# Kernel optimization log

Hardware: AMD Instinct MI355X
Metric: run time of the kernel (lower is better)

The kernel has to match this reference:

```python
import jax, jax.numpy as jnp
import numpy as np

NEG_SLOPE = 0.2  # PyG GATConv default LeakyReLU slope
NUM_GRAPHS = 64


def gat_layer(x, src, dst, W, a_src, a_dst, b, concat):
    """PyG GATConv (eval mode, add_self_loops=True).
    x: [N, F_in]; W: [F_in, H*C]; a_src,a_dst: [H, C]; b: [H*C] or [C].
    """
    N = x.shape[0]
    H, C = a_src.shape
    h = (x @ W).reshape(N, H, C)                      # [N, H, C]
    # add self-loops
    loop = jnp.arange(N, dtype=src.dtype)
    s = jnp.concatenate([src, loop])                  # [E+N]
    d = jnp.concatenate([dst, loop])
    al_s = jnp.einsum('nhc,hc->nh', h, a_src)         # [N, H]
    al_d = jnp.einsum('nhc,hc->nh', h, a_dst)
    e = jax.nn.leaky_relu(al_s[s] + al_d[d], NEG_SLOPE)   # [E+N, H]
    # segment softmax over incoming edges per destination node
    m = jax.ops.segment_max(e, d, num_segments=N)     # [N, H]
    ex = jnp.exp(e - m[d])
    denom = jax.ops.segment_sum(ex, d, num_segments=N)
    alpha = ex / denom[d]                             # [E+N, H]
    msg = h[s] * alpha[:, :, None]                    # [E+N, H, C]
    out = jax.ops.segment_sum(msg, d, num_segments=N) # [N, H, C]
    out = out.reshape(N, H * C) if concat else out.mean(axis=1)
    return out + b


def setup_inputs() -> dict:
    key = jax.random.key(0)
    ks = jax.random.split(key, 16)
    N, E, F_in, Hid, Out = 50000, 800000, 128, 64, 10
    x = jax.random.normal(ks[0], (N, F_in), dtype=jnp.float32)
    edge_index = jax.random.randint(ks[1], (2, E), 0, N, dtype=jnp.int32)
    batch = jnp.sort(jax.random.randint(ks[2], (N,), 0, NUM_GRAPHS, dtype=jnp.int32))

    def glorot(k, shape):
        fan = shape[0] + shape[-1]
        return jax.random.normal(k, shape, dtype=jnp.float32) * np.sqrt(2.0 / fan)

    H1 = 8
    params = dict(
        W1=glorot(ks[3], (F_in, H1 * Hid)), a1_src=glorot(ks[4], (H1, Hid)),
        a1_dst=glorot(ks[5], (H1, Hid)), b1=jnp.zeros((H1 * Hid,), jnp.float32),
        W2=glorot(ks[6], (H1 * Hid, Hid)), a2_src=glorot(ks[7], (1, Hid)),
        a2_dst=glorot(ks[8], (1, Hid)), b2=jnp.zeros((Hid,), jnp.float32),
        W3=glorot(ks[9], (Hid, Hid)), a3_src=glorot(ks[10], (1, Hid)),
        a3_dst=glorot(ks[11], (1, Hid)), b3=jnp.zeros((Hid,), jnp.float32),
        fc_W=glorot(ks[12], (Hid, Out)), fc_b=jnp.zeros((Out,), jnp.float32),
    )
    return dict(x=x, edge_index=edge_index, batch=batch, **params)


def reference(x, edge_index, batch,
              W1, a1_src, a1_dst, b1,
              W2, a2_src, a2_dst, b2,
              W3, a3_src, a3_dst, b3,
              fc_W, fc_b):
    src, dst = edge_index[0], edge_index[1]
    # dropout is a no-op in eval mode
    h = jax.nn.elu(gat_layer(x, src, dst, W1, a1_src, a1_dst, b1, concat=True))
    h = jax.nn.elu(gat_layer(h, src, dst, W2, a2_src, a2_dst, b2, concat=False))
    h = jax.nn.elu(gat_layer(h, src, dst, W3, a3_src, a3_dst, b3, concat=False))
    # global mean pool over graphs
    sums = jax.ops.segment_sum(h, batch, num_segments=NUM_GRAPHS)
    cnts = jax.ops.segment_sum(jnp.ones((h.shape[0], 1), h.dtype), batch,
                               num_segments=NUM_GRAPHS)
    pooled = sums / jnp.maximum(cnts, 1.0)
    return pooled @ fc_W + fc_b
```

## Files before the change

kernel.cpp:

```cpp
#include <hip/hip_runtime.h>
#include <hip/hip_bf16.h>
#include <cstdint>

#define NEG_SLOPE 0.2f

typedef __attribute__((ext_vector_type(8))) short bf16x8;
typedef __attribute__((ext_vector_type(4))) float f32x4;

__device__ __forceinline__ float bf2f(uint32_t u) {
  union { float f; uint32_t i; } v;
  v.i = u << 16;
  return v.f;
}
__device__ __forceinline__ float lo16(uint32_t u) {
  union { float f; uint32_t i; } v;
  v.i = u << 16;
  return v.f;
}
__device__ __forceinline__ float hi16(uint32_t u) {
  union { float f; uint32_t i; } v;
  v.i = u & 0xffff0000u;
  return v.f;
}
__device__ __forceinline__ ushort f2bf(float f) {
  union { float f; uint32_t i; } v;
  v.f = f;
  uint32_t r = v.i + 0x7FFF + ((v.i >> 16) & 1);
  return (ushort)(r >> 16);
}

__global__ void prep_kernel(const float4* __restrict__ x,
                            uint2* __restrict__ x_bf, int n_x4,
                            const float* __restrict__ W1,
                            ushort* __restrict__ W1T,
                            const float* __restrict__ W2,
                            ushort* __restrict__ W2T,
                            const float* __restrict__ W3,
                            ushort* __restrict__ W3T,
                            const int* __restrict__ dst, int* __restrict__ cnt,
                            const float* __restrict__ a1s,
                            const float* __restrict__ a1d,
                            float* __restrict__ at_s, float* __restrict__ at_d,
                            int E) {
  int i = blockIdx.x * 256 + threadIdx.x;
  const int r0 = n_x4;
  const int r1 = r0 + 512 * 128;
  const int r2 = r1 + 64 * 512;
  const int r3 = r2 + 64 * 64;
  const int r4 = r3 + E;
  const int r5 = r4 + 1024;
  const int r6 = r5 + 1024;
  if (i < r0) {
    float4 v = x[i];
    uint2 o;
    o.x = (uint32_t)f2bf(v.x) | ((uint32_t)f2bf(v.y) << 16);
    o.y = (uint32_t)f2bf(v.z) | ((uint32_t)f2bf(v.w) << 16);
    x_bf[i] = o;
  } else if (i < r1) {
    int idx = i - r0;
    int n = idx >> 7, k = idx & 127;
    W1T[idx] = f2bf(W1[(size_t)k * 512 + n]);
  } else if (i < r2) {
    int idx = i - r1;
    int n = idx >> 9, k = idx & 511;
    W2T[idx] = f2bf(W2[(size_t)k * 64 + n]);
  } else if (i < r3) {
    int idx = i - r2;
    int n = idx >> 6, k = idx & 63;
    W3T[idx] = f2bf(W3[(size_t)k * 64 + n]);
  } else if (i < r4) {
    atomicAdd(&cnt[dst[i - r3]], 1);
  } else if (i < r5) {
    int idx = i - r4;
    int k = idx >> 3, h = idx & 7;
    float a = 0.f;
    for (int c = 0; c < 64; ++c)
      a = fmaf(W1[(size_t)k * 512 + h * 64 + c], a1s[h * 64 + c], a);
    at_s[idx] = a;
  } else if (i < r6) {
    int idx = i - r5;
    int k = idx >> 3, h = idx & 7;
    float a = 0.f;
    for (int c = 0; c < 64; ++c)
      a = fmaf(W1[(size_t)k * 512 + h * 64 + c], a1d[h * 64 + c], a);
    at_d[idx] = a;
  }
}

__global__ __launch_bounds__(256) void algemm_kernel(
    const ushort* __restrict__ x_bf, const float* __restrict__ at_s,
    const float* __restrict__ at_d, float* __restrict__ al_s,
    float* __restrict__ al_d, int Nn) {
  const int n = blockIdx.x * 256 + threadIdx.x;
  if (n >= Nn) return;
  float as8[8] = {}, ad8[8] = {};
  const ushort* xp = x_bf + (size_t)n * 128;
  for (int k0 = 0; k0 < 128; k0 += 8) {
    const uint4 xw = *(const uint4*)(xp + k0);
    const uint32_t ww0 = xw.x, ww1 = xw.y, ww2 = xw.z, ww3 = xw.w;
    float xv[8];
    xv[0] = lo16(ww0); xv[1] = hi16(ww0);
    xv[2] = lo16(ww1); xv[3] = hi16(ww1);
    xv[4] = lo16(ww2); xv[5] = hi16(ww2);
    xv[6] = lo16(ww3); xv[7] = hi16(ww3);
#pragma unroll
    for (int t = 0; t < 8; ++t) {
      const int k = k0 + t;
#pragma unroll
      for (int h = 0; h < 8; ++h) {
        as8[h] = fmaf(xv[t], at_s[k * 8 + h], as8[h]);
        ad8[h] = fmaf(xv[t], at_d[k * 8 + h], ad8[h]);
      }
    }
  }
  float4* ps = (float4*)(al_s + (size_t)n * 8);
  ps[0] = make_float4(as8[0], as8[1], as8[2], as8[3]);
  ps[1] = make_float4(as8[4], as8[5], as8[6], as8[7]);
  float4* pd = (float4*)(al_d + (size_t)n * 8);
  pd[0] = make_float4(ad8[0], ad8[1], ad8[2], ad8[3]);
  pd[1] = make_float4(ad8[4], ad8[5], ad8[6], ad8[7]);
}

__global__ __launch_bounds__(256) void gemm_n64_al(
    const ushort* __restrict__ A, const ushort* __restrict__ BT,
    ushort* __restrict__ C, const float* __restrict__ asrc,
    const float* __restrict__ adst, float* __restrict__ al_s,
    float* __restrict__ al_d, int M, int K) {
  const int wave = threadIdx.x >> 6;
  const int lane = threadIdx.x & 63;
  const int rt = blockIdx.y * 4 + wave;
  const int r0 = rt * 16;
  if (r0 >= M) return;
  const int l15 = lane & 15, q = lane >> 4;
  const ushort* Ap = A + (size_t)(r0 + l15) * K + q * 8;
  f32x4 acc[4] = {};
  for (int k0 = 0; k0 < K; k0 += 32) {
    bf16x8 a = *(const bf16x8*)(Ap + k0);
#pragma unroll
    for (int j = 0; j < 4; ++j) {
      const bf16x8 b =
          *(const bf16x8*)(BT + (size_t)(j * 16 + l15) * K + q * 8 + k0);
      acc[j] = __builtin_amdgcn_mfma_f32_16x16x32_bf16(a, b, acc[j], 0, 0, 0);
    }
  }
#pragma unroll
  for (int j = 0; j < 4; ++j)
#pragma unroll
    for (int r = 0; r < 4; ++r) {
      int row = r0 + q * 4 + r;
      C[(size_t)row * 64 + j * 16 + l15] = f2bf(acc[j][r]);
    }
  float als_p[4] = {0.f, 0.f, 0.f, 0.f};
  float ald_p[4] = {0.f, 0.f, 0.f, 0.f};
#pragma unroll
  for (int j = 0; j < 4; ++j) {
    float wsc = asrc[j * 16 + l15];
    float wdc = adst[j * 16 + l15];
#pragma unroll
    for (int r = 0; r < 4; ++r) {
      als_p[r] = fmaf(acc[j][r], wsc, als_p[r]);
      ald_p[r] = fmaf(acc[j][r], wdc, ald_p[r]);
    }
  }
#pragma unroll
  for (int r = 0; r < 4; ++r) {
    float vs = als_p[r], vd = ald_p[r];
#pragma unroll
    for (int off = 1; off < 16; off <<= 1) {
      vs += __shfl_xor(vs, off);
      vd += __shfl_xor(vd, off);
    }
    if (l15 == 0) {
      int row = r0 + q * 4 + r;
      al_s[row] = vs;
      al_d[row] = vd;
    }
  }
}

__global__ __launch_bounds__(256) void gemm1h_kernel(
    const ushort* __restrict__ A, const ushort* __restrict__ BT,
    const float* __restrict__ b1, ushort* __restrict__ C, int M) {
  const int wave = threadIdx.x >> 6;
  const int lane = threadIdx.x & 63;
  const int rt = blockIdx.y * 4 + wave;
  const int r0 = rt * 16;
  if (r0 >= M) return;
  const int hd = blockIdx.x;
  const int l15 = lane & 15, q = lane >> 4;
  const ushort* Ap = A + (size_t)(r0 + l15) * 1024 + hd * 128 + q * 8;
  f32x4 acc[4] = {};
  for (int k0 = 0; k0 < 128; k0 += 32) {
    bf16x8 a = *(const bf16x8*)(Ap + k0);
#pragma unroll
    for (int j = 0; j < 4; ++j) {
      const bf16x8 b = *(const bf16x8*)(BT + (size_t)(hd * 64 + j * 16 + l15) * 128 +
                                        q * 8 + k0);
      acc[j] = __builtin_amdgcn_mfma_f32_16x16x32_bf16(a, b, acc[j], 0, 0, 0);
    }
  }
#pragma unroll
  for (int j = 0; j < 4; ++j)
#pragma unroll
    for (int r = 0; r < 4; ++r) {
      const int row = r0 + q * 4 + r;
      const int col = hd * 64 + j * 16 + l15;
      float v = acc[j][r] + b1[col];
      v = (v > 0.f) ? v : __expf(v) - 1.f;
      C[(size_t)row * 512 + col] = f2bf(v);
    }
}

__global__ void scan_block(const int* __restrict__ in, int* __restrict__ out,
                           int* __restrict__ bsum, int n) {
  __shared__ int sm[256];
  int gid = blockIdx.x * 256 + threadIdx.x;
  int v = (gid < n) ? in[gid] : 0;
  sm[threadIdx.x] = v;
  __syncthreads();
  for (int off = 1; off < 256; off <<= 1) {
    int t = (threadIdx.x >= off) ? sm[threadIdx.x - off] : 0;
    __syncthreads();
    sm[threadIdx.x] += t;
    __syncthreads();
  }
  if (gid < n) out[gid] = sm[threadIdx.x];
  if (threadIdx.x == 255) bsum[blockIdx.x] = sm[255];
}

__global__ void scan_final2(const int* __restrict__ inc,
                            const int* __restrict__ bsum,
                            int* __restrict__ indptr, int* __restrict__ fill,
                            int n) {
  __shared__ int sm[256];
  const int t = threadIdx.x, bx = blockIdx.x;
  sm[t] = (t < bx) ? bsum[t] : 0;
  __syncthreads();
  for (int off = 128; off; off >>= 1) {
    if (t < off) sm[t] += sm[t + off];
    __syncthreads();
  }
  const int prefix = sm[0];
  int gid = bx * 256 + t;
  if (gid < n) {
    int val = inc[gid] + prefix;
    indptr[gid + 1] = val;
    fill[gid + 1] = val;
  }
  if (gid == 0) {
    indptr[0] = 0;
    fill[0] = 0;
  }
}

__global__ void scatter_kernel(const int* __restrict__ src,
                               const int* __restrict__ dst,
                               int* __restrict__ fill,
                               int* __restrict__ csr_src, int E) {
  int e = blockIdx.x * 256 + threadIdx.x;
  if (e < E) {
    int pos = atomicAdd(&fill[dst[e]], 1);
    csr_src[pos] = src[e];
  }
}

__global__ __launch_bounds__(256) void attn1x_kernel(
    const int* __restrict__ indptr, const int* __restrict__ csr_src,
    const float* __restrict__ al_s, const float* __restrict__ al_d,
    const ushort* __restrict__ x_bf, ushort* __restrict__ agg, int Nn) {
  __shared__ float u_sm[4][64 * 8];
  __shared__ int s_sm[4][64];
  const int wv = threadIdx.x >> 6;
  const int l = threadIdx.x & 63;
  const int w = (blockIdx.x * 256 + threadIdx.x) >> 6;
  if (w >= Nn) return;
  const int d = w;
  const int start = indptr[d];
  const int deg = indptr[d + 1] - start;
  const int total = deg + 1;
  const float4 ad0 = *(const float4*)(al_d + (size_t)d * 8);
  const float4 ad1 = *(const float4*)(al_d + (size_t)d * 8 + 4);
  const ushort* xcol = x_bf + l * 2;

  float acc0[8] = {};
  float acc1[8] = {};
  float den8[8] = {};
  float* usm = u_sm[wv];
  int* ssm = s_sm[wv];

  for (int e0 = 0; e0 < total; e0 += 64) {
    const int e = e0 + l;
    int s_l = d;
    float u8[8] = {};
    if (e < total) {
      s_l = (e < deg) ? csr_src[start + e] : d;
      const float4 s0 = *(const float4*)(al_s + (size_t)s_l * 8);
      const float4 s1 = *(const float4*)(al_s + (size_t)s_l * 8 + 4);
      float vv[8];
      vv[0] = s0.x + ad0.x; vv[1] = s0.y + ad0.y;
      vv[2] = s0.z + ad0.z; vv[3] = s0.w + ad0.w;
      vv[4] = s1.x + ad1.x; vv[5] = s1.y + ad1.y;
      vv[6] = s1.z + ad1.z; vv[7] = s1.w + ad1.w;
#pragma unroll
      for (int k = 0; k < 8; ++k) {
        float v = fmaxf(vv[k], NEG_SLOPE * vv[k]);
        u8[k] = __expf(v);
        den8[k] += u8[k];
      }
    }
    ssm[l] = s_l;
    ((float4*)(usm + l * 8))[0] = make_float4(u8[0], u8[1], u8[2], u8[3]);
    ((float4*)(usm + l * 8))[1] = make_float4(u8[4], u8[5], u8[6], u8[7]);

    const int ne = min(64, total - e0);
#pragma unroll 4
    for (int j = 0; j < ne; ++j) {
      const int s = ssm[j];
      const float4 ua = *((const float4*)(usm + j * 8));
      const float4 ub = *((const float4*)(usm + j * 8) + 1);
      const uint32_t wx = *(const uint32_t*)(xcol + (size_t)s * 128);
      const float xlo = lo16(wx);
      const float xhi = hi16(wx);
      acc0[0] = fmaf(ua.x, xlo, acc0[0]); acc1[0] = fmaf(ua.x, xhi, acc1[0]);
      acc0[1] = fmaf(ua.y, xlo, acc0[1]); acc1[1] = fmaf(ua.y, xhi, acc1[1]);
      acc0[2] = fmaf(ua.z, xlo, acc0[2]); acc1[2] = fmaf(ua.z, xhi, acc1[2]);
      acc0[3] = fmaf(ua.w, xlo, acc0[3]); acc1[3] = fmaf(ua.w, xhi, acc1[3]);
      acc0[4] = fmaf(ub.x, xlo, acc0[4]); acc1[4] = fmaf(ub.x, xhi, acc1[4]);
      acc0[5] = fmaf(ub.y, xlo, acc0[5]); acc1[5] = fmaf(ub.y, xhi, acc1[5]);
      acc0[6] = fmaf(ub.z, xlo, acc0[6]); acc1[6] = fmaf(ub.z, xhi, acc1[6]);
      acc0[7] = fmaf(ub.w, xlo, acc0[7]); acc1[7] = fmaf(ub.w, xhi, acc1[7]);
    }
  }
#pragma unroll
  for (int k = 0; k < 8; ++k) {
#pragma unroll
    for (int off = 1; off < 64; off <<= 1) den8[k] += __shfl_xor(den8[k], off);
  }
  ushort* op = agg + (size_t)d * 1024 + l * 2;
#pragma unroll
  for (int h = 0; h < 8; ++h) {
    const float inv = 1.f / den8[h];
    const uint32_t st = (uint32_t)f2bf(acc0[h] * inv) |
                        ((uint32_t)f2bf(acc1[h] * inv) << 16);
    *(uint32_t*)(op + h * 128) = st;
  }
}

__global__ __launch_bounds__(256) void attn_h1_kernel(
    const int* __restrict__ indptr, const int* __restrict__ csr_src,
    const float* __restrict__ al_s, const float* __restrict__ al_d,
    const ushort* __restrict__ hin, const float* __restrict__ bias,
    ushort* __restrict__ outp, int Nn) {
  const int w = (blockIdx.x * 256 + threadIdx.x) >> 6;
  const int l = threadIdx.x & 63;
  if (w >= Nn) return;
  const int d = w;
  const int start = indptr[d];
  const int deg = indptr[d + 1] - start;
  const int total = deg + 1;
  const int t = l >> 3;
  const int c8 = l & 7;
  const float ald = al_d[d];
  const ushort* hl = hin + c8 * 8;

  float acc[8] = {0.f, 0.f, 0.f, 0.f, 0.f, 0.f, 0.f, 0.f};
  float den = 0.f;

  for (int e0 = 0; e0 < total; e0 += 64) {
    const int e = e0 + l;
    int s_l = d;
    float u_l = 0.f;
    if (e < total) {
      s_l = (e < deg) ? csr_src[start + e] : d;
      float v = al_s[s_l] + ald;
      v = fmaxf(v, NEG_SLOPE * v);
      u_l = __expf(v);
      den += u_l;
    }
    const int ne = min(64, total - e0);
    int su0 = __shfl(s_l, t);
    float uv0 = __shfl(u_l, t);
    uint4 h0 = *(const uint4*)(hl + (size_t)su0 * 64);
    int j = 0;
    for (; j + 8 < ne; j += 8) {
      const int su1 = __shfl(s_l, j + 8 + t);
      const float uv1 = __shfl(u_l, j + 8 + t);
      const uint4 h1v = *(const uint4*)(hl + (size_t)su1 * 64);
      acc[0] = fmaf(uv0, lo16(h0.x), acc[0]);
      acc[1] = fmaf(uv0, hi16(h0.x), acc[1]);
      acc[2] = fmaf(uv0, lo16(h0.y), acc[2]);
      acc[3] = fmaf(uv0, hi16(h0.y), acc[3]);
      acc[4] = fmaf(uv0, lo16(h0.z), acc[4]);
      acc[5] = fmaf(uv0, hi16(h0.z), acc[5]);
      acc[6] = fmaf(uv0, lo16(h0.w), acc[6]);
      acc[7] = fmaf(uv0, hi16(h0.w), acc[7]);
      uv0 = uv1;
      h0 = h1v;
    }
    acc[0] = fmaf(uv0, lo16(h0.x), acc[0]);
    acc[1] = fmaf(uv0, hi16(h0.x), acc[1]);
    acc[2] = fmaf(uv0, lo16(h0.y), acc[2]);
    acc[3] = fmaf(uv0, hi16(h0.y), acc[3]);
    acc[4] = fmaf(uv0, lo16(h0.z), acc[4]);
    acc[5] = fmaf(uv0, hi16(h0.z), acc[5]);
    acc[6] = fmaf(uv0, lo16(h0.w), acc[6]);
    acc[7] = fmaf(uv0, hi16(h0.w), acc[7]);
  }
#pragma unroll
  for (int k = 0; k < 8; ++k) {
    acc[k] += __shfl_xor(acc[k], 8);
    acc[k] += __shfl_xor(acc[k], 16);
    acc[k] += __shfl_xor(acc[k], 32);
  }
#pragma unroll
  for (int off = 32; off; off >>= 1) den += __shfl_xor(den, off);
  const float inv = 1.f / den;
  if (l < 8) {
    float o[8];
#pragma unroll
    for (int k = 0; k < 8; ++k) {
      float v = acc[k] * inv + bias[l * 8 + k];
      o[k] = (v > 0.f) ? v : __expf(v) - 1.f;
    }
    uint4 st;
    st.x = (uint32_t)f2bf(o[0]) | ((uint32_t)f2bf(o[1]) << 16);
    st.y = (uint32_t)f2bf(o[2]) | ((uint32_t)f2bf(o[3]) << 16);
    st.z = (uint32_t)f2bf(o[4]) | ((uint32_t)f2bf(o[5]) << 16);
    st.w = (uint32_t)f2bf(o[6]) | ((uint32_t)f2bf(o[7]) << 16);
    *(uint4*)(outp + (size_t)d * 64 + l * 8) = st;
  }
}

__global__ __launch_bounds__(256) void pool_fc_kernel(
    const ushort* __restrict__ out3, const int* __restrict__ batch, int Nn,
    const float* __restrict__ fcW, const float* __restrict__ fcb,
    float* __restrict__ out) {
  __shared__ int bnds[2];
  __shared__ float sm[4 * 64];
  __shared__ float pm[64];
  const int tid = threadIdx.x;
  const int g = blockIdx.x;
  if (tid < 2) {
    int target = g + tid;
    int lo = 0, hi = Nn;
    while (lo < hi) {
      int mid = (lo + hi) >> 1;
      if (batch[mid] < target) lo = mid + 1; else hi = mid;
    }
    bnds[tid] = lo;
  }
  __syncthreads();
  const int lb = bnds[0], ub = bnds[1];

  const int ro = tid >> 3, c8 = tid & 7;
  float acc[8] = {0.f, 0.f, 0.f, 0.f, 0.f, 0.f, 0.f, 0.f};
  for (int r = lb + ro; r < ub; r += 32) {
    const uint4 hh4 = *(const uint4*)(out3 + (size_t)r * 64 + c8 * 8);
    acc[0] += lo16(hh4.x);
    acc[1] += hi16(hh4.x);
    acc[2] += lo16(hh4.y);
    acc[3] += hi16(hh4.y);
    acc[4] += lo16(hh4.z);
    acc[5] += hi16(hh4.z);
    acc[6] += lo16(hh4.w);
    acc[7] += hi16(hh4.w);
  }
#pragma unroll
  for (int k = 0; k < 8; ++k) {
    acc[k] += __shfl_xor(acc[k], 8);
    acc[k] += __shfl_xor(acc[k], 16);
    acc[k] += __shfl_xor(acc[k], 32);
  }
  const int wv = tid >> 6, ll = tid & 63;
  if (ll < 8) {
#pragma unroll
    for (int k = 0; k < 8; ++k) sm[wv * 64 + ll * 8 + k] = acc[k];
  }
  __syncthreads();
  if (tid < 64) {
    float tot = sm[tid] + sm[64 + tid] + sm[128 + tid] + sm[192 + tid];
    pm[tid] = tot / fmaxf((float)(ub - lb), 1.f);
  }
  __syncthreads();
  if (tid < 10) {
    float a = fcb[tid];
    for (int c = 0; c < 64; ++c) a = fmaf(pm[c], fcW[c * 10 + tid], a);
    out[g * 10 + tid] = a;
  }
}

extern "C" void kernel_launch(void* const* d_in, const int* in_sizes, int n_in,
                              void* d_out, int out_size, void* d_ws,
                              size_t ws_size, hipStream_t stream) {
  const float* x = (const float*)d_in[0];
  const int* ei = (const int*)d_in[1];
  const int* batch = (const int*)d_in[2];
  const float* W1 = (const float*)d_in[3];
  const float* a1s = (const float*)d_in[4];
  const float* a1d = (const float*)d_in[5];
  const float* b1 = (const float*)d_in[6];
  const float* W2 = (const float*)d_in[7];
  const float* a2s = (const float*)d_in[8];
  const float* a2d = (const float*)d_in[9];
  const float* b2 = (const float*)d_in[10];
  const float* W3 = (const float*)d_in[11];
  const float* a3s = (const float*)d_in[12];
  const float* a3d = (const float*)d_in[13];
  const float* b3 = (const float*)d_in[14];
  const float* fcW = (const float*)d_in[15];
  const float* fcb = (const float*)d_in[16];
  float* out = (float*)d_out;

  const int N = in_sizes[0] / 128;
  const int E = in_sizes[1] / 2;
  const int* srcp = ei;
  const int* dstp = ei + E;

  char* ws = (char*)d_ws;
  size_t off = 0;
  auto alloc = [&](size_t bytes) -> void* {
    off = (off + 255) & ~(size_t)255;
    void* p = ws + off;
    off += bytes;
    return p;
  };
  ushort* x_bf = (ushort*)alloc((size_t)N * 128 * 2);
  ushort* W1T = (ushort*)alloc(512 * 128 * 2);
  ushort* W2T = (ushort*)alloc(64 * 512 * 2);
  ushort* W3T = (ushort*)alloc(64 * 64 * 2);
  float* at_s = (float*)alloc(128 * 8 * 4);
  float* at_d = (float*)alloc(128 * 8 * 4);
  ushort* agg = (ushort*)alloc((size_t)N * 1024 * 2);
  ushort* out1 = (ushort*)alloc((size_t)N * 512 * 2);
  ushort* hreg = (ushort*)alloc((size_t)4 * N * 64 * 2);
  float* al_s1 = (float*)alloc((size_t)N * 8 * 4);
  float* al_d1 = (float*)alloc((size_t)N * 8 * 4);
  float* al_s2 = (float*)alloc((size_t)N * 4);
  float* al_d2 = (float*)alloc((size_t)N * 4);
  float* al_s3 = (float*)alloc((size_t)N * 4);
  float* al_d3 = (float*)alloc((size_t)N * 4);
  int* cnt = (int*)alloc((size_t)N * 4);
  int* fill = (int*)alloc((size_t)(N + 1) * 4);
  int* indptr = (int*)alloc((size_t)(N + 1) * 4);
  int* csr = (int*)alloc((size_t)E * 4);
  int* incbuf = (int*)alloc((size_t)N * 4);
  int* bsum = (int*)alloc(1024 * 4);

  ushort* h2 = hreg;
  ushort* out2 = hreg + (size_t)N * 64;
  ushort* h3 = hreg + (size_t)2 * N * 64;
  ushort* out3 = hreg + (size_t)3 * N * 64;

  hipMemsetAsync(cnt, 0, (size_t)N * 4, stream);

  const int scan_blocks = (N + 255) / 256;
  const int row_blocks = (N / 16 + 3) / 4;

  const int n_x4 = N * 128 / 4;
  const int prep_total = n_x4 + 512 * 128 + 64 * 512 + 64 * 64 + E + 2048;
  prep_kernel<<<(prep_total + 255) / 256, 256, 0, stream>>>(
      (const float4*)x, (uint2*)x_bf, n_x4, W1, W1T, W2, W2T, W3, W3T, dstp,
      cnt, a1s, a1d, at_s, at_d, E);

  algemm_kernel<<<(N + 255) / 256, 256, 0, stream>>>(x_bf, at_s, at_d, al_s1,
                                                     al_d1, N);
  scan_block<<<scan_blocks, 256, 0, stream>>>(cnt, incbuf, bsum, N);
  scan_final2<<<scan_blocks, 256, 0, stream>>>(incbuf, bsum, indptr, fill, N);
  scatter_kernel<<<(E + 255) / 256, 256, 0, stream>>>(srcp, dstp, fill, csr, E);

  attn1x_kernel<<<(N + 3) / 4, 256, 0, stream>>>(indptr, csr, al_s1, al_d1,
                                                 x_bf, agg, N);
  gemm1h_kernel<<<dim3(8, row_blocks), 256, 0, stream>>>(agg, W1T, b1, out1, N);

  gemm_n64_al<<<dim3(1, row_blocks), 256, 0, stream>>>(out1, W2T, h2, a2s, a2d,
                                                       al_s2, al_d2, N, 512);
  attn_h1_kernel<<<(N + 3) / 4, 256, 0, stream>>>(indptr, csr, al_s2, al_d2, h2,
                                                  b2, out2, N);

  gemm_n64_al<<<dim3(1, row_blocks), 256, 0, stream>>>(out2, W3T, h3, a3s, a3d,
                                                       al_s3, al_d3, N, 64);
  attn_h1_kernel<<<(N + 3) / 4, 256, 0, stream>>>(indptr, csr, al_s3, al_d3, h3,
                                                  b3, out3, N);

  pool_fc_kernel<<<64, 256, 0, stream>>>(out3, batch, N, fcW, fcb, out);
}
```

Before: 484.2 us.

## Fuse layer-1 output GEMM with layer-2 projection through LDS; batch gather loads

Merges the layer-1 head projection GEMM (with bias and ELU) and the layer-2 projection GEMM with its attention logits into one kernel. Each 16-row tile of layer-1 output is staged in shared memory instead of being written to and re-read from global memory, which removes a 50000x512 bf16 round trip and one launch. Separately, the layer-1 aggregation inner loop now issues eight independent source-row gathers before doing the FMAs, to get more memory-level parallelism. The costs are a 16-row block granularity with more LDS use and barriers, W2T being re-read by every block, and higher register pressure in the gather loop.

```diff
diff --git a/kernel.cpp b/kernel.cpp
--- a/kernel.cpp
+++ b/kernel.cpp
@@ -178,37 +178,81 @@
   }
 }
 
-__global__ __launch_bounds__(256) void gemm1h_kernel(
-    const ushort* __restrict__ A, const ushort* __restrict__ BT,
-    const float* __restrict__ b1, ushort* __restrict__ C, int M) {
-  const int wave = threadIdx.x >> 6;
+__global__ __launch_bounds__(256) void gemm12_kernel(
+    const ushort* __restrict__ agg, const ushort* __restrict__ W1T,
+    const float* __restrict__ b1, const ushort* __restrict__ W2T,
+    const float* __restrict__ a2s, const float* __restrict__ a2d,
+    ushort* __restrict__ h2, float* __restrict__ al_s,
+    float* __restrict__ al_d, int M) {
+  __shared__ ushort o1t[16][520];
+  __shared__ float als_sm[4][16];
+  __shared__ float ald_sm[4][16];
+  const int w = threadIdx.x >> 6;
   const int lane = threadIdx.x & 63;
-  const int rt = blockIdx.y * 4 + wave;
-  const int r0 = rt * 16;
-  if (r0 >= M) return;
-  const int hd = blockIdx.x;
   const int l15 = lane & 15, q = lane >> 4;
-  const ushort* Ap = A + (size_t)(r0 + l15) * 1024 + hd * 128 + q * 8;
-  f32x4 acc[4] = {};
-  for (int k0 = 0; k0 < 128; k0 += 32) {
-    bf16x8 a = *(const bf16x8*)(Ap + k0);
-#pragma unroll
-    for (int j = 0; j < 4; ++j) {
-      const bf16x8 b = *(const bf16x8*)(BT + (size_t)(hd * 64 + j * 16 + l15) * 128 +
-                                        q * 8 + k0);
-      acc[j] = __builtin_amdgcn_mfma_f32_16x16x32_bf16(a, b, acc[j], 0, 0, 0);
-    }
-  }
-#pragma unroll
-  for (int j = 0; j < 4; ++j)
-#pragma unroll
-    for (int r = 0; r < 4; ++r) {
-      const int row = r0 + q * 4 + r;
-      const int col = hd * 64 + j * 16 + l15;
-      float v = acc[j][r] + b1[col];
-      v = (v > 0.f) ? v : __expf(v) - 1.f;
-      C[(size_t)row * 512 + col] = f2bf(v);
-    }
+  const int r0 = blockIdx.x * 16;
+  const int rrd = min(r0 + l15, M - 1);
+
+#pragma unroll
+  for (int hi = 0; hi < 2; ++hi) {
+    const int hd = w * 2 + hi;
+    const ushort* Ap = agg + (size_t)rrd * 1024 + hd * 128 + q * 8;
+    f32x4 acc[4] = {};
+    for (int k0 = 0; k0 < 128; k0 += 32) {
+      bf16x8 a = *(const bf16x8*)(Ap + k0);
+#pragma unroll
+      for (int j = 0; j < 4; ++j) {
+        const bf16x8 b = *(const bf16x8*)(W1T +
+            (size_t)(hd * 64 + j * 16 + l15) * 128 + q * 8 + k0);
+        acc[j] = __builtin_amdgcn_mfma_f32_16x16x32_bf16(a, b, acc[j], 0, 0, 0);
+      }
+    }
+#pragma unroll
+    for (int j = 0; j < 4; ++j)
+#pragma unroll
+      for (int r = 0; r < 4; ++r) {
+        const int row = q * 4 + r;
+        const int col = hd * 64 + j * 16 + l15;
+        float v = acc[j][r] + b1[col];
+        v = (v > 0.f) ? v : __expf(v) - 1.f;
+        o1t[row][col] = f2bf(v);
+      }
+  }
+  __syncthreads();
+
+  f32x4 acc2 = {};
+  for (int k0 = 0; k0 < 512; k0 += 32) {
+    const bf16x8 a = *(const bf16x8*)(&o1t[l15][k0 + q * 8]);
+    const bf16x8 b = *(const bf16x8*)(W2T +
+        (size_t)(w * 16 + l15) * 512 + q * 8 + k0);
+    acc2 = __builtin_amdgcn_mfma_f32_16x16x32_bf16(a, b, acc2, 0, 0, 0);
+  }
+  const float wsc = a2s[w * 16 + l15];
+  const float wdc = a2d[w * 16 + l15];
+#pragma unroll
+  for (int r = 0; r < 4; ++r) {
+    const int row = r0 + q * 4 + r;
+    if (row < M) h2[(size_t)row * 64 + w * 16 + l15] = f2bf(acc2[r]);
+    float vs = acc2[r] * wsc, vd = acc2[r] * wdc;
+#pragma unroll
+    for (int off = 1; off < 16; off <<= 1) {
+      vs += __shfl_xor(vs, off);
+      vd += __shfl_xor(vd, off);
+    }
+    if (l15 == 0) {
+      als_sm[w][q * 4 + r] = vs;
+      ald_sm[w][q * 4 + r] = vd;
+    }
+  }
+  __syncthreads();
+  if (threadIdx.x < 16) {
+    const int row = r0 + threadIdx.x;
+    if (row < M) {
+      const int t = threadIdx.x;
+      al_s[row] = als_sm[0][t] + als_sm[1][t] + als_sm[2][t] + als_sm[3][t];
+      al_d[row] = ald_sm[0][t] + ald_sm[1][t] + ald_sm[2][t] + ald_sm[3][t];
+    }
+  }
 }
 
 __global__ void scan_block(const int* __restrict__ in, int* __restrict__ out,
@@ -313,8 +357,32 @@
     ((float4*)(usm + l * 8))[1] = make_float4(u8[4], u8[5], u8[6], u8[7]);
 
     const int ne = min(64, total - e0);
-#pragma unroll 4
-    for (int j = 0; j < ne; ++j) {
+    int j = 0;
+    for (; j + 8 <= ne; j += 8) {
+      const int4 sa = *(const int4*)(ssm + j);
+      const int4 sb = *(const int4*)(ssm + j + 4);
+      const int sv[8] = {sa.x, sa.y, sa.z, sa.w, sb.x, sb.y, sb.z, sb.w};
+      uint32_t wx[8];
+#pragma unroll
+      for (int t = 0; t < 8; ++t)
+        wx[t] = *(const uint32_t*)(xcol + (size_t)sv[t] * 128);
+#pragma unroll
+      for (int t = 0; t < 8; ++t) {
+        const float4 ua = *((const float4*)(usm + (j + t) * 8));
+        const float4 ub = *((const float4*)(usm + (j + t) * 8) + 1);
+        const float xlo = lo16(wx[t]);
+        const float xhi = hi16(wx[t]);
+        acc0[0] = fmaf(ua.x, xlo, acc0[0]); acc1[0] = fmaf(ua.x, xhi, acc1[0]);
+        acc0[1] = fmaf(ua.y, xlo, acc0[1]); acc1[1] = fmaf(ua.y, xhi, acc1[1]);
+        acc0[2] = fmaf(ua.z, xlo, acc0[2]); acc1[2] = fmaf(ua.z, xhi, acc1[2]);
+        acc0[3] = fmaf(ua.w, xlo, acc0[3]); acc1[3] = fmaf(ua.w, xhi, acc1[3]);
+        acc0[4] = fmaf(ub.x, xlo, acc0[4]); acc1[4] = fmaf(ub.x, xhi, acc1[4]);
+        acc0[5] = fmaf(ub.y, xlo, acc0[5]); acc1[5] = fmaf(ub.y, xhi, acc1[5]);
+        acc0[6] = fmaf(ub.z, xlo, acc0[6]); acc1[6] = fmaf(ub.z, xhi, acc1[6]);
+        acc0[7] = fmaf(ub.w, xlo, acc0[7]); acc1[7] = fmaf(ub.w, xhi, acc1[7]);
+      }
+    }
+    for (; j < ne; ++j) {
       const int s = ssm[j];
       const float4 ua = *((const float4*)(usm + j * 8));
       const float4 ub = *((const float4*)(usm + j * 8) + 1);
@@ -531,7 +599,6 @@
   float* at_s = (float*)alloc(128 * 8 * 4);
   float* at_d = (float*)alloc(128 * 8 * 4);
   ushort* agg = (ushort*)alloc((size_t)N * 1024 * 2);
-  ushort* out1 = (ushort*)alloc((size_t)N * 512 * 2);
   ushort* hreg = (ushort*)alloc((size_t)4 * N * 64 * 2);
   float* al_s1 = (float*)alloc((size_t)N * 8 * 4);
   float* al_d1 = (float*)alloc((size_t)N * 8 * 4);
@@ -555,6 +622,7 @@
 
   const int scan_blocks = (N + 255) / 256;
   const int row_blocks = (N / 16 + 3) / 4;
+  const int tile_blocks = (N + 15) / 16;
 
   const int n_x4 = N * 128 / 4;
   const int prep_total = n_x4 + 512 * 128 + 64 * 512 + 64 * 64 + E + 2048;
@@ -570,10 +638,8 @@
 
   attn1x_kernel<<<(N + 3) / 4, 256, 0, stream>>>(indptr, csr, al_s1, al_d1,
                                                  x_bf, agg, N);
-  gemm1h_kernel<<<dim3(8, row_blocks), 256, 0, stream>>>(agg, W1T, b1, out1, N);
-
-  gemm_n64_al<<<dim3(1, row_blocks), 256, 0, stream>>>(out1, W2T, h2, a2s, a2d,
-                                                       al_s2, al_d2, N, 512);
+  gemm12_kernel<<<tile_blocks, 256, 0, stream>>>(agg, W1T, b1, W2T, a2s, a2d,
+                                                 h2, al_s2, al_d2, N);
   attn_h1_kernel<<<(N + 3) / 4, 256, 0, stream>>>(indptr, csr, al_s2, al_d2, h2,
                                                   b2, out2, N);
 
```

Result: faster. 447.9 us (-7.5%).
